# Kernel tuning notes

Measured on AMD Instinct MI355X. Metric: run time of the kernel, lower is better.

The kernel has to match this reference:

```python
import jax, jax.numpy as jnp
import numpy as np

N_NODES = 100000
N_EDGES = 3200000
IN_F = 128
HID = 128


def setup_inputs() -> dict:
    key = jax.random.key(0)
    ks = jax.random.split(key, 6)
    features = jax.random.normal(ks[0], (N_NODES, IN_F), dtype=jnp.float32)
    edge_index = jax.random.randint(ks[1], (2, N_EDGES), 0, N_NODES, dtype=jnp.int64)
    # Glorot-ish scaled weights
    W1 = jax.random.normal(ks[2], (IN_F, HID), dtype=jnp.float32) / np.sqrt(IN_F)
    b1 = jnp.zeros((HID,), dtype=jnp.float32)
    W2 = jax.random.normal(ks[3], (HID, HID), dtype=jnp.float32) / np.sqrt(HID)
    b2 = jnp.zeros((HID,), dtype=jnp.float32)
    prelu_a = jnp.full((HID,), 0.25, dtype=jnp.float32)  # nn.PReLU default init
    return {"features": features, "edge_index": edge_index,
            "W1": W1, "b1": b1, "W2": W2, "b2": b2, "prelu_a": prelu_a}


def _prelu(x, a):
    return jnp.where(x >= 0, x, a[None, :] * x)


def _graph_conv(x, W, b, a, src, dst, dout_is, din_is):
    # DGL GraphConv, norm='both': src-normalize, SpMM aggregate, dst-normalize,
    # dense transform, bias, activation.
    h = x * dout_is[:, None]                                   # [N, F]
    m = jax.ops.segment_sum(h[src], dst, num_segments=N_NODES)  # gather + scatter-add
    m = m * din_is[:, None]
    m = m @ W + b[None, :]
    return _prelu(m, a)


def reference(features, edge_index, W1, b1, W2, b2, prelu_a):
    src, dst = edge_index[0], edge_index[1]
    ones = jnp.ones((N_EDGES,), dtype=jnp.float32)
    deg_out = jax.ops.segment_sum(ones, src, num_segments=N_NODES)
    deg_in = jax.ops.segment_sum(ones, dst, num_segments=N_NODES)
    dout_is = jax.lax.rsqrt(jnp.clip(deg_out, 1.0))
    din_is = jax.lax.rsqrt(jnp.clip(deg_in, 1.0))
    h = _graph_conv(features, W1, b1, prelu_a, src, dst, dout_is, din_is)
    h = _graph_conv(h, W2, b2, prelu_a, src, dst, dout_is, din_is)
    return h
```

## Files before the change

### kernel.cpp

```cpp
#include <hip/hip_runtime.h>
#include <hip/hip_fp16.h>

#define NN 100000
#define EE 3200000
#define FF 128

#define NBUK 391
#define CAP 12288
#define CH_A 8192
#define NB_A ((EE + CH_A - 1) / CH_A)

typedef _Float16 f16x8 __attribute__((ext_vector_type(8)));
typedef float f32x4 __attribute__((ext_vector_type(4)));
typedef int vint4 __attribute__((ext_vector_type(4)));
typedef float vfloat4 __attribute__((ext_vector_type(4)));

__global__ __launch_bounds__(256) void k_bin(const int* __restrict__ ei,
                                             int* __restrict__ dcur_g,
                                             int* __restrict__ scur_g,
                                             unsigned int* __restrict__ binned,
                                             int* __restrict__ src_binned) {
  __shared__ int hd[NBUK];
  __shared__ int hs[NBUK];
  __shared__ int cd[NBUK];
  __shared__ int cs[NBUK];
  int tid = threadIdx.x;
  for (int t = tid; t < NBUK; t += 256) { hd[t] = 0; hs[t] = 0; }
  __syncthreads();
  int base = blockIdx.x * CH_A;
  const int* dst = ei + EE;
#pragma unroll
  for (int k = 0; k < CH_A / 256; ++k) {
    int e = base + k * 256 + tid;
    if (e < EE) {
      atomicAdd(&hs[ei[e] >> 8], 1);
      atomicAdd(&hd[dst[e] >> 8], 1);
    }
  }
  __syncthreads();
  for (int t = tid; t < NBUK; t += 256) {
    cd[t] = (hd[t] > 0) ? atomicAdd(&dcur_g[t], hd[t]) : 0;
    cs[t] = (hs[t] > 0) ? atomicAdd(&scur_g[t], hs[t]) : 0;
  }
  __syncthreads();
#pragma unroll
  for (int k = 0; k < CH_A / 256; ++k) {
    int e = base + k * 256 + tid;
    if (e < EE) {
      int s = ei[e];
      int d = dst[e];
      int db = d >> 8;
      int dpos = atomicAdd(&cd[db], 1);
      binned[(size_t)db * CAP + dpos] = ((unsigned int)(d & 255) << 24) | (unsigned int)s;
      int sb = s >> 8;
      int spos = atomicAdd(&cs[sb], 1);
      src_binned[(size_t)sb * CAP + spos] = s;
    }
  }
}

__global__ __launch_bounds__(256) void k_csr(const unsigned int* __restrict__ binned,
                                             const int* __restrict__ dcnt,
                                             int2* __restrict__ offs2,
                                             float* __restrict__ din_is,
                                             int* __restrict__ csr_src) {
  __shared__ unsigned int recs[CAP];
  __shared__ int h[256];
  __shared__ int sa[256];
  __shared__ int cur[256];
  int tid = threadIdx.x;
  int b = blockIdx.x;
  int gbeg = b * CAP;
  int cnt = dcnt[b];

  for (int t = tid; t < cnt; t += 256) recs[t] = binned[gbeg + t];
  h[tid] = 0;
  __syncthreads();
  for (int t = tid; t < cnt; t += 256) atomicAdd(&h[recs[t] >> 24], 1);
  __syncthreads();
  sa[tid] = h[tid];
  __syncthreads();
  for (int off = 1; off < 256; off <<= 1) {
    int v = (tid >= off) ? sa[tid - off] : 0;
    __syncthreads();
    sa[tid] += v;
    __syncthreads();
  }
  int deg = h[tid];
  int excl = sa[tid] - deg;
  cur[tid] = gbeg + excl;
  int node = (b << 8) + tid;
  if (node < NN) {
    offs2[node] = make_int2(gbeg + excl, gbeg + excl + deg);
    int d = deg < 1 ? 1 : deg;
    din_is[node] = rsqrtf((float)d);
  }
  __syncthreads();
  for (int t = tid; t < cnt; t += 256) {
    unsigned int r = recs[t];
    int pos = atomicAdd(&cur[r >> 24], 1);
    csr_src[pos] = (int)(r & 0xFFFFFFu);
  }
}

__global__ __launch_bounds__(256) void k_srchist(const int* __restrict__ src_binned,
                                                 const int* __restrict__ scnt,
                                                 float* __restrict__ dout_is) {
  __shared__ int h[256];
  int tid = threadIdx.x;
  int b = blockIdx.x;
  int src0 = b << 8;
  int gbeg = b * CAP;
  int cnt = scnt[b];
  h[tid] = 0;
  __syncthreads();
  for (int t = tid; t < cnt; t += 256) {
    atomicAdd(&h[src_binned[gbeg + t] - src0], 1);
  }
  __syncthreads();
  int node = src0 + tid;
  if (node < NN) {
    int d = h[tid]; if (d < 1) d = 1;
    dout_is[node] = rsqrtf((float)d);
  }
}

__global__ __launch_bounds__(256) void k_wprep(const float* __restrict__ W,
                                               __half* __restrict__ Wt) {
  int t = blockIdx.x * blockDim.x + threadIdx.x;
  if (t >= FF * FF) return;
  int n = t >> 7, k = t & 127;
  Wt[n * FF + k] = __float2half(W[k * FF + n]);
}

__global__ __launch_bounds__(256) void k_prescale_h(const float* __restrict__ x,
                                                    const float* __restrict__ dout_is,
                                                    __half* __restrict__ xh) {
  int t = blockIdx.x * blockDim.x + threadIdx.x;
  if (t >= NN * (FF / 4)) return;
  int node = t >> 5;
  float sc = dout_is[node];
  vfloat4 v = __builtin_nontemporal_load((const vfloat4*)x + t);
  union { __half2 h[2]; uint2 u; } p;
  p.h[0] = __floats2half2_rn(v.x * sc, v.y * sc);
  p.h[1] = __floats2half2_rn(v.z * sc, v.w * sc);
  ((uint2*)xh)[t] = p.u;
}

__global__ __launch_bounds__(256) void k_agg(const __half* __restrict__ xh,
                                             const float* __restrict__ din_is,
                                             const int2* __restrict__ offs2,
                                             const int* __restrict__ csr_src,
                                             __half* __restrict__ outh) {
  int gid = blockIdx.x * blockDim.x + threadIdx.x;
  int node = gid >> 6;
  int lane = threadIdx.x & 63;
  if (node >= NN) return;
  int2 oo = offs2[node];
  int beg = oo.x, end = oo.y;
  float ax = 0.f, ay = 0.f, bx = 0.f, by = 0.f;
  float cx = 0.f, cy = 0.f, dx = 0.f, dy = 0.f;
  int e = beg;
  for (; e < end && (e & 3); ++e) {
    int s = csr_src[e];
    float2 v = __half22float2(((const __half2*)(xh + (size_t)s * FF))[lane]);
    ax += v.x; ay += v.y;
  }
  for (; e + 16 <= end; e += 16) {
    vint4 i0 = __builtin_nontemporal_load((const vint4*)(csr_src + e));
    vint4 i1 = __builtin_nontemporal_load((const vint4*)(csr_src + e + 4));
    vint4 i2 = __builtin_nontemporal_load((const vint4*)(csr_src + e + 8));
    vint4 i3 = __builtin_nontemporal_load((const vint4*)(csr_src + e + 12));
    float2 v0 = __half22float2(((const __half2*)(xh + (size_t)i0.x * FF))[lane]);
    float2 v1 = __half22float2(((const __half2*)(xh + (size_t)i0.y * FF))[lane]);
    float2 v2 = __half22float2(((const __half2*)(xh + (size_t)i0.z * FF))[lane]);
    float2 v3 = __half22float2(((const __half2*)(xh + (size_t)i0.w * FF))[lane]);
    float2 v4 = __half22float2(((const __half2*)(xh + (size_t)i1.x * FF))[lane]);
    float2 v5 = __half22float2(((const __half2*)(xh + (size_t)i1.y * FF))[lane]);
    float2 v6 = __half22float2(((const __half2*)(xh + (size_t)i1.z * FF))[lane]);
    float2 v7 = __half22float2(((const __half2*)(xh + (size_t)i1.w * FF))[lane]);
    float2 v8 = __half22float2(((const __half2*)(xh + (size_t)i2.x * FF))[lane]);
    float2 v9 = __half22float2(((const __half2*)(xh + (size_t)i2.y * FF))[lane]);
    float2 va = __half22float2(((const __half2*)(xh + (size_t)i2.z * FF))[lane]);
    float2 vb = __half22float2(((const __half2*)(xh + (size_t)i2.w * FF))[lane]);
    float2 vc = __half22float2(((const __half2*)(xh + (size_t)i3.x * FF))[lane]);
    float2 vd = __half22float2(((const __half2*)(xh + (size_t)i3.y * FF))[lane]);
    float2 ve = __half22float2(((const __half2*)(xh + (size_t)i3.z * FF))[lane]);
    float2 vf = __half22float2(((const __half2*)(xh + (size_t)i3.w * FF))[lane]);
    ax += v0.x; ay += v0.y; bx += v1.x; by += v1.y;
    cx += v2.x; cy += v2.y; dx += v3.x; dy += v3.y;
    ax += v4.x; ay += v4.y; bx += v5.x; by += v5.y;
    cx += v6.x; cy += v6.y; dx += v7.x; dy += v7.y;
    ax += v8.x; ay += v8.y; bx += v9.x; by += v9.y;
    cx += va.x; cy += va.y; dx += vb.x; dy += vb.y;
    ax += vc.x; ay += vc.y; bx += vd.x; by += vd.y;
    cx += ve.x; cy += ve.y; dx += vf.x; dy += vf.y;
  }
  for (; e + 4 <= end; e += 4) {
    vint4 i0 = __builtin_nontemporal_load((const vint4*)(csr_src + e));
    float2 v0 = __half22float2(((const __half2*)(xh + (size_t)i0.x * FF))[lane]);
    float2 v1 = __half22float2(((const __half2*)(xh + (size_t)i0.y * FF))[lane]);
    float2 v2 = __half22float2(((const __half2*)(xh + (size_t)i0.z * FF))[lane]);
    float2 v3 = __half22float2(((const __half2*)(xh + (size_t)i0.w * FF))[lane]);
    ax += v0.x; ay += v0.y; bx += v1.x; by += v1.y;
    cx += v2.x; cy += v2.y; dx += v3.x; dy += v3.y;
  }
  for (; e < end; ++e) {
    int s = csr_src[e];
    float2 v = __half22float2(((const __half2*)(xh + (size_t)s * FF))[lane]);
    ax += v.x; ay += v.y;
  }
  float di = din_is[node];
  __half2 r = __floats2half2_rn((ax + bx + cx + dx) * di, (ay + by + cy + dy) * di);
  ((__half2*)(outh + (size_t)node * FF))[lane] = r;
}

__global__ __launch_bounds__(256) void k_gemm_mfma(const __half* __restrict__ X,
                                                   const __half* __restrict__ Wt,
                                                   const float* __restrict__ bias,
                                                   const float* __restrict__ pa,
                                                   const float* __restrict__ postscale,
                                                   int out_half,
                                                   float* __restrict__ outf,
                                                   __half* __restrict__ outh) {
  __shared__ __half Xs[64][FF + 8];
  __shared__ __half Ws[FF][FF + 8];
  int tid = threadIdx.x;
  int row0 = blockIdx.x * 64;

  for (int t = tid; t < 64 * 16; t += 256) {
    int r = t >> 4, c8 = (t & 15) * 8;
    int row = row0 + r;
    uint4 v = make_uint4(0, 0, 0, 0);
    if (row < NN) v = *(const uint4*)(X + (size_t)row * FF + c8);
    *(uint4*)&Xs[r][c8] = v;
  }
  for (int t = tid; t < FF * 16; t += 256) {
    int r = t >> 4, c8 = (t & 15) * 8;
    uint4 v = *(const uint4*)(Wt + r * FF + c8);
    *(uint4*)&Ws[r][c8] = v;
  }
  __syncthreads();

  int wid = tid >> 6;
  int lane = tid & 63;
  int l15 = lane & 15;
  int g = lane >> 4;
  int arow = wid * 16 + l15;

  f32x4 acc[8];
#pragma unroll
  for (int n = 0; n < 8; ++n) acc[n] = (f32x4){0.f, 0.f, 0.f, 0.f};

  union FU { uint2 u[2]; f16x8 v; };
#pragma unroll
  for (int kk = 0; kk < 4; ++kk) {
    int kb = kk * 32;
    FU a;
    a.u[0] = *(const uint2*)&Xs[arow][kb + 4 * g];
    a.u[1] = *(const uint2*)&Xs[arow][kb + 16 + 4 * g];
#pragma unroll
    for (int n = 0; n < 8; ++n) {
      FU b;
      int wr = n * 16 + l15;
      b.u[0] = *(const uint2*)&Ws[wr][kb + 4 * g];
      b.u[1] = *(const uint2*)&Ws[wr][kb + 16 + 4 * g];
      acc[n] = __builtin_amdgcn_mfma_f32_16x16x32_f16(a.v, b.v, acc[n], 0, 0, 0);
    }
  }

#pragma unroll
  for (int n = 0; n < 8; ++n) {
    int col = n * 16 + l15;
    float bb = bias[col];
    float aa = pa[col];
#pragma unroll
    for (int j = 0; j < 4; ++j) {
      int row = row0 + wid * 16 + g * 4 + j;
      if (row < NN) {
        float v = acc[n][j] + bb;
        v = v >= 0.f ? v : aa * v;
        if (out_half) {
          v *= postscale[row];
          outh[(size_t)row * FF + col] = __float2half(v);
        } else {
          outf[(size_t)row * FF + col] = v;
        }
      }
    }
  }
}

extern "C" void kernel_launch(void* const* d_in, const int* in_sizes, int n_in,
                              void* d_out, int out_size, void* d_ws, size_t ws_size,
                              hipStream_t stream) {
  const float* features = (const float*)d_in[0];
  const int*   ei       = (const int*)d_in[1];
  const float* W1       = (const float*)d_in[2];
  const float* b1       = (const float*)d_in[3];
  const float* W2       = (const float*)d_in[4];
  const float* b2       = (const float*)d_in[5];
  const float* pa       = (const float*)d_in[6];
  float* out = (float*)d_out;

  char* ws = (char*)d_ws;
  size_t off = 0;
  auto alloc = [&](size_t bytes) -> void* {
    void* p = ws + off;
    off += (bytes + 255) & ~(size_t)255;
    return p;
  };
  int*    cur     = (int*)alloc((size_t)2 * NBUK * 4);
  int*    dcur    = cur;
  int*    scur    = cur + NBUK;
  float*  dout_is = (float*)alloc((size_t)NN * 4);
  float*  din_is  = (float*)alloc((size_t)NN * 4);
  int2*   offs2   = (int2*)alloc((size_t)NN * 8);
  int*    csr_src = (int*)alloc((size_t)NBUK * CAP * 4);
  unsigned int* binned = (unsigned int*)alloc((size_t)NBUK * CAP * 4);
  int*    src_binned   = (int*)alloc((size_t)NBUK * CAP * 4);
  __half* tmp_h   = (__half*)alloc((size_t)NN * FF * 2);
  __half* w1t     = (__half*)alloc((size_t)FF * FF * 2);
  __half* w2t     = (__half*)alloc((size_t)FF * FF * 2);
  __half* xh      = (__half*)binned;

  (void)hipMemsetAsync(cur, 0, (size_t)2 * NBUK * 4, stream);

  k_bin<<<NB_A, 256, 0, stream>>>(ei, dcur, scur, binned, src_binned);
  k_csr<<<NBUK, 256, 0, stream>>>(binned, dcur, offs2, din_is, csr_src);
  k_srchist<<<NBUK, 256, 0, stream>>>(src_binned, scur, dout_is);

  k_wprep<<<(FF * FF + 255) / 256, 256, 0, stream>>>(W1, w1t);
  k_wprep<<<(FF * FF + 255) / 256, 256, 0, stream>>>(W2, w2t);

  k_prescale_h<<<(NN * FF / 4 + 255) / 256, 256, 0, stream>>>(features, dout_is, xh);
  k_agg<<<NN / 4, 256, 0, stream>>>(xh, din_is, offs2, csr_src, tmp_h);
  k_gemm_mfma<<<(NN + 63) / 64, 256, 0, stream>>>(tmp_h, w1t, b1, pa, dout_is, 1, nullptr, xh);

  k_agg<<<NN / 4, 256, 0, stream>>>(xh, din_is, offs2, csr_src, tmp_h);
  k_gemm_mfma<<<(NN + 63) / 64, 256, 0, stream>>>(tmp_h, w2t, b2, pa, nullptr, 0, out, nullptr);
}
```

Measured before the change: 446.3 us.

## Merge weight prep, shrink aggregation unroll, double GEMM row tile, drop nontemporal loads

Combines the two weight-transpose launches into one kernel. The aggregation loop unroll drops from 16 to 8 edges with two accumulator pairs instead of four, and regular loads replace the nontemporal ones there and in the prescale kernel. The MFMA GEMM now handles 128 rows per block, so each warp computes two 16-row tiles and reuses each B fragment across both. The aim is to cut launch overhead and LDS weight reloads, at the cost of less memory-level parallelism in the gather and fewer GEMM blocks.

Result: faster. 434.7 us (-2.6%).

```diff
diff --git a/kernel.cpp b/kernel.cpp
--- a/kernel.cpp
+++ b/kernel.cpp
@@ -12,8 +12,6 @@
 
 typedef _Float16 f16x8 __attribute__((ext_vector_type(8)));
 typedef float f32x4 __attribute__((ext_vector_type(4)));
-typedef int vint4 __attribute__((ext_vector_type(4)));
-typedef float vfloat4 __attribute__((ext_vector_type(4)));
 
 __global__ __launch_bounds__(256) void k_bin(const int* __restrict__ ei,
                                              int* __restrict__ dcur_g,
@@ -125,11 +123,17 @@
   }
 }
 
-__global__ __launch_bounds__(256) void k_wprep(const float* __restrict__ W,
-                                               __half* __restrict__ Wt) {
+__global__ __launch_bounds__(256) void k_wprep2(const float* __restrict__ W1,
+                                                const float* __restrict__ W2,
+                                                __half* __restrict__ w1t,
+                                                __half* __restrict__ w2t) {
   int t = blockIdx.x * blockDim.x + threadIdx.x;
-  if (t >= FF * FF) return;
-  int n = t >> 7, k = t & 127;
+  int which = t >= FF * FF;
+  int u = t - which * FF * FF;
+  if (u >= FF * FF) return;
+  int n = u >> 7, k = u & 127;
+  const float* W = which ? W2 : W1;
+  __half* Wt = which ? w2t : w1t;
   Wt[n * FF + k] = __float2half(W[k * FF + n]);
 }
 
@@ -140,7 +144,7 @@
   if (t >= NN * (FF / 4)) return;
   int node = t >> 5;
   float sc = dout_is[node];
-  vfloat4 v = __builtin_nontemporal_load((const vfloat4*)x + t);
+  float4 v = ((const float4*)x)[t];
   union { __half2 h[2]; uint2 u; } p;
   p.h[0] = __floats2half2_rn(v.x * sc, v.y * sc);
   p.h[1] = __floats2half2_rn(v.z * sc, v.w * sc);
@@ -159,18 +163,15 @@
   int2 oo = offs2[node];
   int beg = oo.x, end = oo.y;
   float ax = 0.f, ay = 0.f, bx = 0.f, by = 0.f;
-  float cx = 0.f, cy = 0.f, dx = 0.f, dy = 0.f;
   int e = beg;
   for (; e < end && (e & 3); ++e) {
     int s = csr_src[e];
     float2 v = __half22float2(((const __half2*)(xh + (size_t)s * FF))[lane]);
     ax += v.x; ay += v.y;
   }
-  for (; e + 16 <= end; e += 16) {
-    vint4 i0 = __builtin_nontemporal_load((const vint4*)(csr_src + e));
-    vint4 i1 = __builtin_nontemporal_load((const vint4*)(csr_src + e + 4));
-    vint4 i2 = __builtin_nontemporal_load((const vint4*)(csr_src + e + 8));
-    vint4 i3 = __builtin_nontemporal_load((const vint4*)(csr_src + e + 12));
+  for (; e + 8 <= end; e += 8) {
+    int4 i0 = *(const int4*)(csr_src + e);
+    int4 i1 = *(const int4*)(csr_src + e + 4);
     float2 v0 = __half22float2(((const __half2*)(xh + (size_t)i0.x * FF))[lane]);
     float2 v1 = __half22float2(((const __half2*)(xh + (size_t)i0.y * FF))[lane]);
     float2 v2 = __half22float2(((const __half2*)(xh + (size_t)i0.z * FF))[lane]);
@@ -179,31 +180,10 @@
     float2 v5 = __half22float2(((const __half2*)(xh + (size_t)i1.y * FF))[lane]);
     float2 v6 = __half22float2(((const __half2*)(xh + (size_t)i1.z * FF))[lane]);
     float2 v7 = __half22float2(((const __half2*)(xh + (size_t)i1.w * FF))[lane]);
-    float2 v8 = __half22float2(((const __half2*)(xh + (size_t)i2.x * FF))[lane]);
-    float2 v9 = __half22float2(((const __half2*)(xh + (size_t)i2.y * FF))[lane]);
-    float2 va = __half22float2(((const __half2*)(xh + (size_t)i2.z * FF))[lane]);
-    float2 vb = __half22float2(((const __half2*)(xh + (size_t)i2.w * FF))[lane]);
-    float2 vc = __half22float2(((const __half2*)(xh + (size_t)i3.x * FF))[lane]);
-    float2 vd = __half22float2(((const __half2*)(xh + (size_t)i3.y * FF))[lane]);
-    float2 ve = __half22float2(((const __half2*)(xh + (size_t)i3.z * FF))[lane]);
-    float2 vf = __half22float2(((const __half2*)(xh + (size_t)i3.w * FF))[lane]);
     ax += v0.x; ay += v0.y; bx += v1.x; by += v1.y;
-    cx += v2.x; cy += v2.y; dx += v3.x; dy += v3.y;
+    ax += v2.x; ay += v2.y; bx += v3.x; by += v3.y;
     ax += v4.x; ay += v4.y; bx += v5.x; by += v5.y;
-    cx += v6.x; cy += v6.y; dx += v7.x; dy += v7.y;
-    ax += v8.x; ay += v8.y; bx += v9.x; by += v9.y;
-    cx += va.x; cy += va.y; dx += vb.x; dy += vb.y;
-    ax += vc.x; ay += vc.y; bx += vd.x; by += vd.y;
-    cx += ve.x; cy += ve.y; dx += vf.x; dy += vf.y;
-  }
-  for (; e + 4 <= end; e += 4) {
-    vint4 i0 = __builtin_nontemporal_load((const vint4*)(csr_src + e));
-    float2 v0 = __half22float2(((const __half2*)(xh + (size_t)i0.x * FF))[lane]);
-    float2 v1 = __half22float2(((const __half2*)(xh + (size_t)i0.y * FF))[lane]);
-    float2 v2 = __half22float2(((const __half2*)(xh + (size_t)i0.z * FF))[lane]);
-    float2 v3 = __half22float2(((const __half2*)(xh + (size_t)i0.w * FF))[lane]);
-    ax += v0.x; ay += v0.y; bx += v1.x; by += v1.y;
-    cx += v2.x; cy += v2.y; dx += v3.x; dy += v3.y;
+    ax += v6.x; ay += v6.y; bx += v7.x; by += v7.y;
   }
   for (; e < end; ++e) {
     int s = csr_src[e];
@@ -211,7 +191,7 @@
     ax += v.x; ay += v.y;
   }
   float di = din_is[node];
-  __half2 r = __floats2half2_rn((ax + bx + cx + dx) * di, (ay + by + cy + dy) * di);
+  __half2 r = __floats2half2_rn((ax + bx) * di, (ay + by) * di);
   ((__half2*)(outh + (size_t)node * FF))[lane] = r;
 }
 
@@ -223,12 +203,12 @@
                                                    int out_half,
                                                    float* __restrict__ outf,
                                                    __half* __restrict__ outh) {
-  __shared__ __half Xs[64][FF + 8];
+  __shared__ __half Xs[128][FF + 8];
   __shared__ __half Ws[FF][FF + 8];
   int tid = threadIdx.x;
-  int row0 = blockIdx.x * 64;
-
-  for (int t = tid; t < 64 * 16; t += 256) {
+  int row0 = blockIdx.x * 128;
+
+  for (int t = tid; t < 128 * 16; t += 256) {
     int r = t >> 4, c8 = (t & 15) * 8;
     int row = row0 + r;
     uint4 v = make_uint4(0, 0, 0, 0);
@@ -246,45 +226,54 @@
   int lane = tid & 63;
   int l15 = lane & 15;
   int g = lane >> 4;
-  int arow = wid * 16 + l15;
-
-  f32x4 acc[8];
-#pragma unroll
-  for (int n = 0; n < 8; ++n) acc[n] = (f32x4){0.f, 0.f, 0.f, 0.f};
+  int arow0 = wid * 16 + l15;
+  int arow1 = 64 + arow0;
+
+  f32x4 acc[2][8];
+#pragma unroll
+  for (int h = 0; h < 2; ++h)
+#pragma unroll
+    for (int n = 0; n < 8; ++n) acc[h][n] = (f32x4){0.f, 0.f, 0.f, 0.f};
 
   union FU { uint2 u[2]; f16x8 v; };
 #pragma unroll
   for (int kk = 0; kk < 4; ++kk) {
     int kb = kk * 32;
-    FU a;
-    a.u[0] = *(const uint2*)&Xs[arow][kb + 4 * g];
-    a.u[1] = *(const uint2*)&Xs[arow][kb + 16 + 4 * g];
+    FU a0, a1;
+    a0.u[0] = *(const uint2*)&Xs[arow0][kb + 4 * g];
+    a0.u[1] = *(const uint2*)&Xs[arow0][kb + 16 + 4 * g];
+    a1.u[0] = *(const uint2*)&Xs[arow1][kb + 4 * g];
+    a1.u[1] = *(const uint2*)&Xs[arow1][kb + 16 + 4 * g];
 #pragma unroll
     for (int n = 0; n < 8; ++n) {
       FU b;
       int wr = n * 16 + l15;
       b.u[0] = *(const uint2*)&Ws[wr][kb + 4 * g];
       b.u[1] = *(const uint2*)&Ws[wr][kb + 16 + 4 * g];
-      acc[n] = __builtin_amdgcn_mfma_f32_16x16x32_f16(a.v, b.v, acc[n], 0, 0, 0);
+      acc[0][n] = __builtin_amdgcn_mfma_f32_16x16x32_f16(a0.v, b.v, acc[0][n], 0, 0, 0);
+      acc[1][n] = __builtin_amdgcn_mfma_f32_16x16x32_f16(a1.v, b.v, acc[1][n], 0, 0, 0);
     }
   }
 
 #pragma unroll
-  for (int n = 0; n < 8; ++n) {
-    int col = n * 16 + l15;
-    float bb = bias[col];
-    float aa = pa[col];
-#pragma unroll
-    for (int j = 0; j < 4; ++j) {
-      int row = row0 + wid * 16 + g * 4 + j;
-      if (row < NN) {
-        float v = acc[n][j] + bb;
-        v = v >= 0.f ? v : aa * v;
-        if (out_half) {
-          v *= postscale[row];
-          outh[(size_t)row * FF + col] = __float2half(v);
-        } else {
-          outf[(size_t)row * FF + col] = v;
+  for (int h = 0; h < 2; ++h) {
+#pragma unroll
+    for (int n = 0; n < 8; ++n) {
+      int col = n * 16 + l15;
+      float bb = bias[col];
+      float aa = pa[col];
+#pragma unroll
+      for (int j = 0; j < 4; ++j) {
+        int row = row0 + h * 64 + wid * 16 + g * 4 + j;
+        if (row < NN) {
+          float v = acc[h][n][j] + bb;
+          v = v >= 0.f ? v : aa * v;
+          if (out_half) {
+            v *= postscale[row];
+            outh[(size_t)row * FF + col] = __float2half(v);
+          } else {
+            outf[(size_t)row * FF + col] = v;
+          }
         }
       }
     }
@@ -330,13 +319,12 @@
   k_csr<<<NBUK, 256, 0, stream>>>(binned, dcur, offs2, din_is, csr_src);
   k_srchist<<<NBUK, 256, 0, stream>>>(src_binned, scur, dout_is);
 
-  k_wprep<<<(FF * FF + 255) / 256, 256, 0, stream>>>(W1, w1t);
-  k_wprep<<<(FF * FF + 255) / 256, 256, 0, stream>>>(W2, w2t);
+  k_wprep2<<<(2 * FF * FF + 255) / 256, 256, 0, stream>>>(W1, W2, w1t, w2t);
 
   k_prescale_h<<<(NN * FF / 4 + 255) / 256, 256, 0, stream>>>(features, dout_is, xh);
   k_agg<<<NN / 4, 256, 0, stream>>>(xh, din_is, offs2, csr_src, tmp_h);
-  k_gemm_mfma<<<(NN + 63) / 64, 256, 0, stream>>>(tmp_h, w1t, b1, pa, dout_is, 1, nullptr, xh);
+  k_gemm_mfma<<<(NN + 127) / 128, 256, 0, stream>>>(tmp_h, w1t, b1, pa, dout_is, 1, nullptr, xh);
 
   k_agg<<<NN / 4, 256, 0, stream>>>(xh, din_is, offs2, csr_src, tmp_h);
-  k_gemm_mfma<<<(NN + 63) / 64, 256, 0, stream>>>(tmp_h, w2t, b2, pa, nullptr, 0, out, nullptr);
-}
+  k_gemm_mfma<<<(NN + 127) / 128, 256, 0, stream>>>(tmp_h, w2t, b2, pa, nullptr, 0, out, nullptr);
+}
```
